# Performance work log

Hardware: AMD Instinct MI355X
Metric: run time of the kernel (lower is better)

Reference implementation:

```python
import jax, jax.numpy as jnp
import numpy as np
import math

B, S, H, NH = 1, 2048, 1024, 16  # batch, seq, hidden, heads


def setup_inputs() -> dict:
    key = jax.random.key(0)
    ks = jax.random.split(key, 12)
    inp = {
        "query": jax.random.normal(ks[0], (B, S, H), dtype=jnp.float32),
        "key": jax.random.normal(ks[1], (B, S, H), dtype=jnp.float32),
        "value": jax.random.normal(ks[2], (B, S, H), dtype=jnp.float32),
        "attention_mask": jax.random.randint(ks[3], (1, 1, S, S), 0, 2, dtype=jnp.int32),
        # torch nn.Linear params: y = x @ W.T + b, W init ~ U(-1/sqrt(H), 1/sqrt(H))
        "Wq": jax.random.uniform(ks[4], (H, H), jnp.float32, -1, 1) / math.sqrt(H),
        "bq": jax.random.uniform(ks[5], (H,), jnp.float32, -1, 1) / math.sqrt(H),
        "Wk": jax.random.uniform(ks[6], (H, H), jnp.float32, -1, 1) / math.sqrt(H),
        "bk": jax.random.uniform(ks[7], (H,), jnp.float32, -1, 1) / math.sqrt(H),
        "Wv": jax.random.uniform(ks[8], (H, H), jnp.float32, -1, 1) / math.sqrt(H),
        "bv": jax.random.uniform(ks[9], (H,), jnp.float32, -1, 1) / math.sqrt(H),
        "Wo": jax.random.uniform(ks[10], (H, H), jnp.float32, -1, 1) / math.sqrt(H),
        "bo": jax.random.uniform(ks[11], (H,), jnp.float32, -1, 1) / math.sqrt(H),
        "head": NH,
        "hidden_size": H,
    }
    return inp


def reference(query, key, value, attention_mask, Wq, bq, Wk, bk, Wv, bv, Wo, bo, head, hidden_size):
    b, s, _ = query.shape
    d_k = hidden_size // head

    def proj(x, W, bias):
        # [b, s, hidden] -> [b, head, s, d_k]
        y = x @ W.T + bias
        return y.reshape(b, s, head, d_k).transpose(0, 2, 1, 3)

    q = proj(query, Wq, bq)
    k = proj(key, Wk, bk)
    v = proj(value, Wv, bv)

    # naive full score matrix, as in the source (scale by sqrt(d_k) = last dim of q)
    scores = jnp.einsum("bhqd,bhkd->bhqk", q, k) / math.sqrt(d_k)
    # faithful quirk: masked positions are set to 0 (not -inf) before softmax
    scores = jnp.where(attention_mask == 0, jnp.zeros((), scores.dtype), scores)
    attn = jax.nn.softmax(scores, axis=-1)

    out = jnp.einsum("bhqk,bhkd->bhqd", attn, v)  # [b, head, s, d_k]
    out = out.transpose(0, 2, 1, 3).reshape(b, s, head * d_k)
    return out @ Wo.T + bo
```

## Files before the change

kernel.cpp:

```cpp
#include <hip/hip_runtime.h>
#include <hip/hip_bf16.h>


#define S_LEN 2048
#define HID   1024
#define NHEAD 16
#define DK    64

typedef unsigned short u16;
typedef __attribute__((ext_vector_type(8))) short bf16x8;
typedef __attribute__((ext_vector_type(4))) short bf16x4;
typedef __attribute__((ext_vector_type(4))) float f32x4;
typedef __attribute__((ext_vector_type(4))) unsigned u32x4;

__device__ __forceinline__ void load16_lds(const void* g, void* l) {
  __builtin_amdgcn_global_load_lds(
      (const __attribute__((address_space(1))) void*)g,
      (__attribute__((address_space(3))) void*)l, 16, 0, 0);
}

__device__ __forceinline__ short bfbits(float x) {
  __hip_bfloat16 h = __float2bfloat16(x);
  return *(short*)&h;
}
__device__ __forceinline__ bf16x8 cvt8(float4 a, float4 b) {
  bf16x8 r;
  r[0] = bfbits(a.x); r[1] = bfbits(a.y); r[2] = bfbits(a.z); r[3] = bfbits(a.w);
  r[4] = bfbits(b.x); r[5] = bfbits(b.y); r[6] = bfbits(b.z); r[7] = bfbits(b.w);
  return r;
}
__device__ __forceinline__ float bf2f(u16 u) {
  unsigned v = (unsigned)u << 16;
  return *(float*)&v;
}

__global__ __launch_bounds__(256) void cvt_kernel(
    const float* __restrict__ q, const float* __restrict__ k,
    const float* __restrict__ v, const float* __restrict__ wq,
    const float* __restrict__ wk, const float* __restrict__ wv,
    const float* __restrict__ wo, u16* __restrict__ Xbf,
    u16* __restrict__ Wbf) {
  const int y = blockIdx.y;
  size_t i = ((size_t)blockIdx.x * 256 + threadIdx.x) * 8;
  const float* src;
  u16* dst;
  size_t n;
  if (y < 3) {
    src = y == 0 ? q : (y == 1 ? k : v);
    dst = Xbf + (size_t)y * (S_LEN * HID);
    n = (size_t)S_LEN * HID;
  } else {
    int w = y - 3;
    src = w == 0 ? wq : (w == 1 ? wk : (w == 2 ? wv : wo));
    dst = Wbf + (size_t)w * (HID * HID);
    n = (size_t)HID * HID;
  }
  if (i >= n) return;
  float4 a = *(const float4*)(src + i);
  float4 b = *(const float4*)(src + i + 4);
  *(bf16x8*)(dst + i) = cvt8(a, b);
}

__global__ __launch_bounds__(256) void pack_mask_kernel(
    const int* __restrict__ mask, unsigned int* __restrict__ bitsT) {
  int idx = blockIdx.x * 256 + threadIdx.x;
  int row = idx & 2047, widx = idx >> 11;
  const int4* p = (const int4*)(mask + (size_t)row * S_LEN + widx * 32);
  unsigned word = 0;
#pragma unroll
  for (int i = 0; i < 8; ++i) {
    int4 v = p[i];
    word |= (unsigned)(v.x != 0) << (i * 4 + 0);
    word |= (unsigned)(v.y != 0) << (i * 4 + 1);
    word |= (unsigned)(v.z != 0) << (i * 4 + 2);
    word |= (unsigned)(v.w != 0) << (i * 4 + 3);
  }
  bitsT[(size_t)widx * S_LEN + row] = word;
}

__global__ __launch_bounds__(256) void gemm_qkv(
    const u16* __restrict__ Xbf, const u16* __restrict__ Wbf,
    const float* __restrict__ bq, const float* __restrict__ bk,
    const float* __restrict__ bv, u16* __restrict__ Qb,
    u16* __restrict__ Kb, u16* __restrict__ Vt) {
  constexpr int Mm = 2048, Nn = 1024, Kk = 1024, NIT = 16;
  const int z = blockIdx.z;
  const u16* A = Xbf + (size_t)z * (S_LEN * HID);
  const u16* W = Wbf + (size_t)z * (HID * HID);
  const float* bias = z == 0 ? bq : (z == 1 ? bk : bv);
  u16* C = z == 0 ? Qb : (z == 1 ? Kb : Vt);
  const float oscale = (z == 0) ? 0.125f * 1.44269504088896f : 1.0f;
  const int transpose = (z == 2);

  const int tid = threadIdx.x, lane = tid & 63, wave = tid >> 6;
  const int q4 = lane >> 4, c16 = lane & 15;
  const int bx = blockIdx.x;
  const int mBase = (bx & 31) * 64;
  const int nBase = (bx >> 5) * 128;
  const int wn = wave * 32;

  __shared__ __align__(16) u16 As[2][2][64 * 32];
  __shared__ __align__(16) u16 Bs[2][2][128 * 32];

  f32x4 acc[4][2] = {};
  const int srow = lane >> 2, se8 = (lane & 3) * 8;

  auto issue = [&](int it, int buf) {
#pragma unroll
    for (int j = 0; j < 2; ++j) {
      int u = wave * 2 + j, h = u >> 2, grp = u & 3;
      load16_lds(A + (size_t)(mBase + grp * 16 + srow) * Kk + it * 64 +
                     h * 32 + se8,
                 &As[buf][h][grp * 512]);
    }
#pragma unroll
    for (int j = 0; j < 4; ++j) {
      int u = wave * 4 + j, h = u >> 3, grp = u & 7;
      load16_lds(W + (size_t)(nBase + grp * 16 + srow) * Kk + it * 64 +
                     h * 32 + se8,
                 &Bs[buf][h][grp * 512]);
    }
  };

  issue(0, 0);
  __syncthreads();

  for (int it = 0; it < NIT; ++it) {
    const int buf = it & 1, nbuf = buf ^ 1;
    if (it + 1 < NIT) issue(it + 1, nbuf);
#pragma unroll
    for (int kk = 0; kk < 2; ++kk) {
      bf16x8 af[4], bfr[2];
#pragma unroll
      for (int t = 0; t < 4; ++t)
        af[t] = *(const bf16x8*)&As[buf][kk][(t * 16 + c16) * 32 + q4 * 8];
#pragma unroll
      for (int t = 0; t < 2; ++t)
        bfr[t] = *(const bf16x8*)&Bs[buf][kk][(wn + t * 16 + c16) * 32 + q4 * 8];
#pragma unroll
      for (int mt = 0; mt < 4; ++mt)
#pragma unroll
        for (int nt = 0; nt < 2; ++nt)
          acc[mt][nt] = __builtin_amdgcn_mfma_f32_16x16x32_bf16(
              af[mt], bfr[nt], acc[mt][nt], 0, 0, 0);
    }
    __syncthreads();
  }

#pragma unroll
  for (int nt = 0; nt < 2; ++nt) {
    int col = nBase + wn + nt * 16 + c16;
    float bv2 = bias[col];
#pragma unroll
    for (int mt = 0; mt < 4; ++mt) {
#pragma unroll
      for (int r = 0; r < 4; ++r) {
        int row = mBase + mt * 16 + q4 * 4 + r;
        float v = (acc[mt][nt][r] + bv2) * oscale;
        if (transpose)
          ((__hip_bfloat16*)C)[(size_t)col * Mm + row] = __float2bfloat16(v);
        else
          ((__hip_bfloat16*)C)[(size_t)row * Nn + col] = __float2bfloat16(v);
      }
    }
  }
}

__global__ __launch_bounds__(512, 4) void attn_kernel(
    const u16* __restrict__ Qb, const u16* __restrict__ Kb,
    const u16* __restrict__ Vt, const unsigned* __restrict__ mbT,
    u16* __restrict__ partOA, u16* __restrict__ partO3,
    float* __restrict__ partL) {
  constexpr int NITA = 8;
  const int qt = blockIdx.x, h = blockIdx.y, zz = blockIdx.z;
  const int tid = threadIdx.x, lane = tid & 63, wave = tid >> 6;
  const int q4 = lane >> 4, c16 = lane & 15;

  __shared__ __align__(16) u16 Ks[2][2][64 * 32];
  __shared__ __align__(16) u16 Vs[2][2][64 * 32];
  __shared__ __align__(16) u16 Ps[8][32 * 72];

  const int q0 = qt * 256 + wave * 32;

  bf16x8 qf[2][2];
#pragma unroll
  for (int m = 0; m < 2; ++m)
#pragma unroll
    for (int kk = 0; kk < 2; ++kk)
      qf[m][kk] = *(const bf16x8*)(Qb + (size_t)(q0 + m * 16 + c16) * HID +
                                   h * DK + kk * 32 + q4 * 8);

  f32x4 o[2][4] = {};
  float l_lane[2][4] = {{}, {}};
  const unsigned mlo = 1u << c16, mhi = mlo << 16;

  const int srow = lane >> 2;
  const int sslot = ((lane & 3) ^ (srow & 3)) * 8;
  const int kvbase = zz * (S_LEN / 4);

  auto issueKV = [&](int it, int buf) {
    const int kv0 = kvbase + it * 64;
#pragma unroll
    for (int j = 0; j < 2; ++j) {
      int i = wave * 2 + j;
      if (i < 8) {
        int half = i >> 2, grp = i & 3;
        load16_lds(Kb + (size_t)(kv0 + grp * 16 + srow) * HID + h * DK +
                       half * 32 + sslot,
                   &Ks[buf][half][grp * 512]);
      } else {
        int ii = i - 8;
        int half = ii >> 2, grp = ii & 3;
        load16_lds(Vt + (size_t)(h * DK + grp * 16 + srow) * S_LEN + kv0 +
                       half * 32 + sslot,
                   &Vs[buf][half][grp * 512]);
      }
    }
  };

  issueKV(0, 0);
  __syncthreads();

  __hip_bfloat16* pw = (__hip_bfloat16*)&Ps[wave][0];

  for (int it = 0; it < NITA; ++it) {
    const int buf = it & 1, nbuf = buf ^ 1;
    if (it + 1 < NITA) issueKV(it + 1, nbuf);

    const unsigned* mr = mbT + (size_t)(zz * 16 + it * 2) * S_LEN + q0 + q4 * 4;
    u32x4 mwa[2][2];
#pragma unroll
    for (int m = 0; m < 2; ++m) {
      mwa[m][0] = *(const u32x4*)(mr + m * 16);
      mwa[m][1] = *(const u32x4*)(mr + S_LEN + m * 16);
    }

#pragma unroll
    for (int nt = 0; nt < 4; ++nt) {
      const int rsw = (nt * 16 + c16) * 32 + ((q4 ^ (c16 & 3)) * 8);
      bf16x8 kf0 = *(const bf16x8*)&Ks[buf][0][rsw];
      bf16x8 kf1 = *(const bf16x8*)&Ks[buf][1][rsw];
#pragma unroll
      for (int m = 0; m < 2; ++m) {
        f32x4 a = {};
        a = __builtin_amdgcn_mfma_f32_16x16x32_bf16(qf[m][0], kf0, a, 0, 0, 0);
        a = __builtin_amdgcn_mfma_f32_16x16x32_bf16(qf[m][1], kf1, a, 0, 0, 0);
#pragma unroll
        for (int r = 0; r < 4; ++r) {
          unsigned word = mwa[m][nt >> 1][r];
          unsigned keep = word & ((nt & 1) ? mhi : mlo);
          float s = keep ? a[r] : 0.0f;
          float p = exp2f(s);
          l_lane[m][r] += p;
          pw[(m * 16 + q4 * 4 + r) * 72 + nt * 16 + c16] = __float2bfloat16(p);
        }
      }
    }

    asm volatile("s_waitcnt lgkmcnt(0)" ::: "memory");

#pragma unroll
    for (int kk = 0; kk < 2; ++kk) {
      bf16x8 pa0 = *(const bf16x8*)&Ps[wave][(c16) * 72 + kk * 32 + q4 * 8];
      bf16x8 pa1 = *(const bf16x8*)&Ps[wave][(16 + c16) * 72 + kk * 32 + q4 * 8];
#pragma unroll
      for (int nt = 0; nt < 4; ++nt) {
        const int rsw = (nt * 16 + c16) * 32 + ((q4 ^ (c16 & 3)) * 8);
        bf16x8 vb = *(const bf16x8*)&Vs[buf][kk][rsw];
        o[0][nt] = __builtin_amdgcn_mfma_f32_16x16x32_bf16(pa0, vb, o[0][nt], 0, 0, 0);
        o[1][nt] = __builtin_amdgcn_mfma_f32_16x16x32_bf16(pa1, vb, o[1][nt], 0, 0, 0);
      }
    }
    __syncthreads();
  }

  u16* pO = (zz < 3) ? (partOA + (size_t)zz * (S_LEN * HID)) : partO3;
#pragma unroll
  for (int m = 0; m < 2; ++m)
#pragma unroll
    for (int r = 0; r < 4; ++r) {
      float s = l_lane[m][r];
#pragma unroll
      for (int d = 1; d < 16; d <<= 1) s += __shfl_xor(s, d);
      int row = q0 + m * 16 + q4 * 4 + r;
#pragma unroll
      for (int nt = 0; nt < 4; ++nt)
        ((__hip_bfloat16*)pO)[(size_t)row * HID + h * DK + nt * 16 + c16] =
            __float2bfloat16(o[m][nt][r]);
      if (c16 == 0)
        partL[((size_t)zz * NHEAD + h) * S_LEN + row] = s;
    }
}

__global__ __launch_bounds__(256) void combine_kernel(
    const u16* __restrict__ pOA, const u16* __restrict__ pO3,
    const float* __restrict__ partL, u16* __restrict__ ctx) {
  size_t idx = ((size_t)blockIdx.x * 256 + threadIdx.x) * 4;
  int row = (int)(idx >> 10);
  int col = (int)(idx & 1023);
  int h = col >> 6;
  float l = 0.0f;
#pragma unroll
  for (int z = 0; z < 4; ++z)
    l += partL[((size_t)z * NHEAD + h) * S_LEN + row];
  float inv = 1.0f / l;
  bf16x4 a0 = *(const bf16x4*)(pOA + idx);
  bf16x4 a1 = *(const bf16x4*)(pOA + (size_t)S_LEN * HID + idx);
  bf16x4 a2 = *(const bf16x4*)(pOA + 2 * (size_t)S_LEN * HID + idx);
  bf16x4 a3 = *(const bf16x4*)(pO3 + idx);
  bf16x4 r;
#pragma unroll
  for (int j = 0; j < 4; ++j) {
    float v = (bf2f((u16)a0[j]) + bf2f((u16)a1[j]) + bf2f((u16)a2[j]) +
               bf2f((u16)a3[j])) * inv;
    r[j] = bfbits(v);
  }
  *(bf16x4*)(ctx + idx) = r;
}

__global__ __launch_bounds__(256) void gemm_out(
    const u16* __restrict__ ctx, const u16* __restrict__ Wo,
    const float* __restrict__ bo, float* __restrict__ out) {
  constexpr int Nn = 1024, Kk = 1024, NIT = 16;
  const int tid = threadIdx.x, lane = tid & 63, wave = tid >> 6;
  const int q4 = lane >> 4, c16 = lane & 15;
  const int bx = blockIdx.x;
  const int mBase = (bx & 63) * 32;
  const int nBase = (bx >> 6) * 128;
  const int wn = wave * 32;

  __shared__ __align__(16) u16 As[2][2][32 * 32];
  __shared__ __align__(16) u16 Bs[2][2][128 * 32];

  f32x4 acc[2][2] = {};
  const int srow = lane >> 2, se8 = (lane & 3) * 8;

  auto issue = [&](int it, int buf) {
    {
      int u = wave, h = u >> 1, grp = u & 1;
      load16_lds(ctx + (size_t)(mBase + grp * 16 + srow) * Kk + it * 64 +
                     h * 32 + se8,
                 &As[buf][h][grp * 512]);
    }
#pragma unroll
    for (int j = 0; j < 4; ++j) {
      int u = wave * 4 + j, h = u >> 3, grp = u & 7;
      load16_lds(Wo + (size_t)(nBase + grp * 16 + srow) * Kk + it * 64 +
                     h * 32 + se8,
                 &Bs[buf][h][grp * 512]);
    }
  };

  issue(0, 0);
  __syncthreads();

  for (int it = 0; it < NIT; ++it) {
    const int buf = it & 1, nbuf = buf ^ 1;
    if (it + 1 < NIT) issue(it + 1, nbuf);
#pragma unroll
    for (int kk = 0; kk < 2; ++kk) {
      bf16x8 af[2], bfr[2];
#pragma unroll
      for (int t = 0; t < 2; ++t)
        af[t] = *(const bf16x8*)&As[buf][kk][(t * 16 + c16) * 32 + q4 * 8];
#pragma unroll
      for (int t = 0; t < 2; ++t)
        bfr[t] = *(const bf16x8*)&Bs[buf][kk][(wn + t * 16 + c16) * 32 + q4 * 8];
#pragma unroll
      for (int mt = 0; mt < 2; ++mt)
#pragma unroll
        for (int nt = 0; nt < 2; ++nt)
          acc[mt][nt] = __builtin_amdgcn_mfma_f32_16x16x32_bf16(
              af[mt], bfr[nt], acc[mt][nt], 0, 0, 0);
    }
    __syncthreads();
  }

#pragma unroll
  for (int nt = 0; nt < 2; ++nt) {
    int col = nBase + wn + nt * 16 + c16;
    float bv = bo[col];
#pragma unroll
    for (int mt = 0; mt < 2; ++mt)
#pragma unroll
      for (int r = 0; r < 4; ++r) {
        int row = mBase + mt * 16 + q4 * 4 + r;
        out[(size_t)row * Nn + col] = acc[mt][nt][r] + bv;
      }
  }
}

extern "C" void kernel_launch(void* const* d_in, const int* in_sizes, int n_in,
                              void* d_out, int out_size, void* d_ws, size_t ws_size,
                              hipStream_t stream) {
  const float* q    = (const float*)d_in[0];
  const float* k    = (const float*)d_in[1];
  const float* v    = (const float*)d_in[2];
  const int*   mask = (const int*)d_in[3];
  const float* Wq = (const float*)d_in[4];
  const float* bq = (const float*)d_in[5];
  const float* Wk = (const float*)d_in[6];
  const float* bk = (const float*)d_in[7];
  const float* Wv = (const float*)d_in[8];
  const float* bv = (const float*)d_in[9];
  const float* Wo = (const float*)d_in[10];
  const float* bo = (const float*)d_in[11];

  const size_t M2 = (size_t)S_LEN * HID;
  const size_t W1 = (size_t)HID * HID;
  const size_t need = (4 * W1 + 3 * M2 + 3 * M2) * 2 +
                      (size_t)S_LEN * 64 * 4 + 2 * NHEAD * S_LEN * 4;
  if (ws_size < need) return;

  u16* Wbf = (u16*)d_ws;
  u16* Xbf = Wbf + 4 * W1;
  u16* Qb = Xbf + 3 * M2;
  u16* Kb = Qb + M2;
  u16* Vt = Kb + M2;
  unsigned* mbits = (unsigned*)(Vt + M2);
  u16* partOA = Xbf;
  u16* partO3 = Wbf;
  float* partL = (float*)(Wbf + 2 * W1);
  u16* ctx = Qb;

  hipLaunchKernelGGL(cvt_kernel, dim3(1024, 7), dim3(256), 0, stream,
                     q, k, v, Wq, Wk, Wv, Wo, Xbf, Wbf);

  hipLaunchKernelGGL(pack_mask_kernel, dim3((S_LEN * (S_LEN / 32)) / 256),
                     dim3(256), 0, stream, mask, mbits);

  hipLaunchKernelGGL(gemm_qkv, dim3(256, 1, 3), dim3(256), 0, stream,
                     Xbf, Wbf, bq, bk, bv, Qb, Kb, Vt);

  hipLaunchKernelGGL(attn_kernel, dim3(S_LEN / 256, NHEAD, 4), dim3(512), 0,
                     stream, Qb, Kb, Vt, mbits, partOA, partO3, partL);

  hipLaunchKernelGGL(combine_kernel, dim3((S_LEN * HID / 4) / 256), dim3(256),
                     0, stream, partOA, partO3, partL, ctx);

  hipLaunchKernelGGL(gemm_out, dim3(512), dim3(256), 0, stream,
                     ctx, Wbf + 3 * W1, bo, (float*)d_out);
}
```

Measured before the change: 227.0 us.

## Swizzle LDS tiles, remap blocks per XCD, pack P stores with permuted V

Changes the LDS XOR swizzle in the QKV, output and attention kernels to key on (row>>1), so 16-byte fragment reads hit fewer bank conflicts. Remaps block indices in all three kernels so blocks on the same XCD share A/W or K/V tiles in that XCD's L2. In attention, the score-to-P write is restructured to emit packed 32-bit bf16 pairs instead of scattered 16-bit stores. To keep that correct, the V^T output of the QKV GEMM is written with a matching interleaved row permutation within each 32-key group. The added index arithmetic and the coupled layout across kernels raise the risk of subtle correctness mismatches.

```diff
diff --git a/kernel.cpp b/kernel.cpp
--- a/kernel.cpp
+++ b/kernel.cpp
@@ -95,29 +95,32 @@
   const int tid = threadIdx.x, lane = tid & 63, wave = tid >> 6;
   const int q4 = lane >> 4, c16 = lane & 15;
   const int bx = blockIdx.x;
-  const int mBase = (bx & 31) * 64;
-  const int nBase = (bx >> 5) * 128;
+  const int xcd = bx & 7, sIdx = bx >> 3;
+  const int mBase = ((xcd >> 1) * 8 + (sIdx & 7)) * 64;
+  const int nBase = ((xcd & 1) * 4 + (sIdx >> 3)) * 128;
   const int wn = wave * 32;
 
   __shared__ __align__(16) u16 As[2][2][64 * 32];
   __shared__ __align__(16) u16 Bs[2][2][128 * 32];
 
   f32x4 acc[4][2] = {};
-  const int srow = lane >> 2, se8 = (lane & 3) * 8;
+  const int srow = lane >> 2;
+  const int sx8 = ((lane & 3) ^ ((srow >> 1) & 3)) * 8;
+  const int rx8 = (q4 ^ ((c16 >> 1) & 3)) * 8;
 
   auto issue = [&](int it, int buf) {
 #pragma unroll
     for (int j = 0; j < 2; ++j) {
       int u = wave * 2 + j, h = u >> 2, grp = u & 3;
       load16_lds(A + (size_t)(mBase + grp * 16 + srow) * Kk + it * 64 +
-                     h * 32 + se8,
+                     h * 32 + sx8,
                  &As[buf][h][grp * 512]);
     }
 #pragma unroll
     for (int j = 0; j < 4; ++j) {
       int u = wave * 4 + j, h = u >> 3, grp = u & 7;
       load16_lds(W + (size_t)(nBase + grp * 16 + srow) * Kk + it * 64 +
-                     h * 32 + se8,
+                     h * 32 + sx8,
                  &Bs[buf][h][grp * 512]);
     }
   };
@@ -133,10 +136,10 @@
       bf16x8 af[4], bfr[2];
 #pragma unroll
       for (int t = 0; t < 4; ++t)
-        af[t] = *(const bf16x8*)&As[buf][kk][(t * 16 + c16) * 32 + q4 * 8];
+        af[t] = *(const bf16x8*)&As[buf][kk][(t * 16 + c16) * 32 + rx8];
 #pragma unroll
       for (int t = 0; t < 2; ++t)
-        bfr[t] = *(const bf16x8*)&Bs[buf][kk][(wn + t * 16 + c16) * 32 + q4 * 8];
+        bfr[t] = *(const bf16x8*)&Bs[buf][kk][(wn + t * 16 + c16) * 32 + rx8];
 #pragma unroll
       for (int mt = 0; mt < 4; ++mt)
 #pragma unroll
@@ -157,10 +160,13 @@
       for (int r = 0; r < 4; ++r) {
         int row = mBase + mt * 16 + q4 * 4 + r;
         float v = (acc[mt][nt][r] + bv2) * oscale;
-        if (transpose)
-          ((__hip_bfloat16*)C)[(size_t)col * Mm + row] = __float2bfloat16(v);
-        else
+        if (transpose) {
+          int vv = row & 31;
+          int rowp = (row & ~31) | (((vv & 15) << 1) | (vv >> 4));
+          ((__hip_bfloat16*)C)[(size_t)col * Mm + rowp] = __float2bfloat16(v);
+        } else {
           ((__hip_bfloat16*)C)[(size_t)row * Nn + col] = __float2bfloat16(v);
+        }
       }
     }
   }
@@ -172,7 +178,9 @@
     u16* __restrict__ partOA, u16* __restrict__ partO3,
     float* __restrict__ partL) {
   constexpr int NITA = 8;
-  const int qt = blockIdx.x, h = blockIdx.y, zz = blockIdx.z;
+  const int lin = blockIdx.x + 8 * (blockIdx.y + 16 * blockIdx.z);
+  const int work = ((lin & 7) << 6) | (lin >> 3);
+  const int qt = work & 7, h = (work >> 3) & 15, zz = work >> 7;
   const int tid = threadIdx.x, lane = tid & 63, wave = tid >> 6;
   const int q4 = lane >> 4, c16 = lane & 15;
 
@@ -195,7 +203,8 @@
   const unsigned mlo = 1u << c16, mhi = mlo << 16;
 
   const int srow = lane >> 2;
-  const int sslot = ((lane & 3) ^ (srow & 3)) * 8;
+  const int sx8 = ((lane & 3) ^ ((srow >> 1) & 3)) * 8;
+  const int rx8 = (q4 ^ ((c16 >> 1) & 3)) * 8;
   const int kvbase = zz * (S_LEN / 4);
 
   auto issueKV = [&](int it, int buf) {
@@ -206,13 +215,13 @@
       if (i < 8) {
         int half = i >> 2, grp = i & 3;
         load16_lds(Kb + (size_t)(kv0 + grp * 16 + srow) * HID + h * DK +
-                       half * 32 + sslot,
+                       half * 32 + sx8,
                    &Ks[buf][half][grp * 512]);
       } else {
         int ii = i - 8;
         int half = ii >> 2, grp = ii & 3;
         load16_lds(Vt + (size_t)(h * DK + grp * 16 + srow) * S_LEN + kv0 +
-                       half * 32 + sslot,
+                       half * 32 + sx8,
                    &Vs[buf][half][grp * 512]);
       }
     }
@@ -221,7 +230,7 @@
   issueKV(0, 0);
   __syncthreads();
 
-  __hip_bfloat16* pw = (__hip_bfloat16*)&Ps[wave][0];
+  u16* pw = &Ps[wave][0];
 
   for (int it = 0; it < NITA; ++it) {
     const int buf = it & 1, nbuf = buf ^ 1;
@@ -235,9 +244,10 @@
       mwa[m][1] = *(const u32x4*)(mr + S_LEN + m * 16);
     }
 
+    f32x4 sv[2][4];
 #pragma unroll
     for (int nt = 0; nt < 4; ++nt) {
-      const int rsw = (nt * 16 + c16) * 32 + ((q4 ^ (c16 & 3)) * 8);
+      const int rsw = (nt * 16 + c16) * 32 + rx8;
       bf16x8 kf0 = *(const bf16x8*)&Ks[buf][0][rsw];
       bf16x8 kf1 = *(const bf16x8*)&Ks[buf][1][rsw];
 #pragma unroll
@@ -245,27 +255,41 @@
         f32x4 a = {};
         a = __builtin_amdgcn_mfma_f32_16x16x32_bf16(qf[m][0], kf0, a, 0, 0, 0);
         a = __builtin_amdgcn_mfma_f32_16x16x32_bf16(qf[m][1], kf1, a, 0, 0, 0);
-#pragma unroll
-        for (int r = 0; r < 4; ++r) {
+        sv[m][nt] = a;
+      }
+    }
+
+#pragma unroll
+    for (int m = 0; m < 2; ++m)
+#pragma unroll
+      for (int r = 0; r < 4; ++r) {
+#pragma unroll
+        for (int nt = 0; nt < 4; ++nt) {
           unsigned word = mwa[m][nt >> 1][r];
           unsigned keep = word & ((nt & 1) ? mhi : mlo);
-          float s = keep ? a[r] : 0.0f;
+          float s = keep ? sv[m][nt][r] : 0.0f;
           float p = exp2f(s);
+          sv[m][nt][r] = p;
           l_lane[m][r] += p;
-          pw[(m * 16 + q4 * 4 + r) * 72 + nt * 16 + c16] = __float2bfloat16(p);
         }
-      }
-    }
+        int prow = m * 16 + q4 * 4 + r;
+#pragma unroll
+        for (int kkp = 0; kkp < 2; ++kkp) {
+          unsigned lo = (unsigned)(u16)bfbits(sv[m][2 * kkp][r]);
+          unsigned hi = (unsigned)(u16)bfbits(sv[m][2 * kkp + 1][r]);
+          *(unsigned*)&pw[prow * 72 + kkp * 32 + c16 * 2] = lo | (hi << 16);
+        }
+      }
 
     asm volatile("s_waitcnt lgkmcnt(0)" ::: "memory");
 
 #pragma unroll
     for (int kk = 0; kk < 2; ++kk) {
-      bf16x8 pa0 = *(const bf16x8*)&Ps[wave][(c16) * 72 + kk * 32 + q4 * 8];
-      bf16x8 pa1 = *(const bf16x8*)&Ps[wave][(16 + c16) * 72 + kk * 32 + q4 * 8];
+      bf16x8 pa0 = *(const bf16x8*)&pw[(c16) * 72 + kk * 32 + q4 * 8];
+      bf16x8 pa1 = *(const bf16x8*)&pw[(16 + c16) * 72 + kk * 32 + q4 * 8];
 #pragma unroll
       for (int nt = 0; nt < 4; ++nt) {
-        const int rsw = (nt * 16 + c16) * 32 + ((q4 ^ (c16 & 3)) * 8);
+        const int rsw = (nt * 16 + c16) * 32 + rx8;
         bf16x8 vb = *(const bf16x8*)&Vs[buf][kk][rsw];
         o[0][nt] = __builtin_amdgcn_mfma_f32_16x16x32_bf16(pa0, vb, o[0][nt], 0, 0, 0);
         o[1][nt] = __builtin_amdgcn_mfma_f32_16x16x32_bf16(pa1, vb, o[1][nt], 0, 0, 0);
@@ -325,28 +349,31 @@
   const int tid = threadIdx.x, lane = tid & 63, wave = tid >> 6;
   const int q4 = lane >> 4, c16 = lane & 15;
   const int bx = blockIdx.x;
-  const int mBase = (bx & 63) * 32;
-  const int nBase = (bx >> 6) * 128;
+  const int xcd = bx & 7, sIdx = bx >> 3;
+  const int mBase = ((xcd >> 1) * 16 + (sIdx & 15)) * 32;
+  const int nBase = ((xcd & 1) * 4 + (sIdx >> 4)) * 128;
   const int wn = wave * 32;
 
   __shared__ __align__(16) u16 As[2][2][32 * 32];
   __shared__ __align__(16) u16 Bs[2][2][128 * 32];
 
   f32x4 acc[2][2] = {};
-  const int srow = lane >> 2, se8 = (lane & 3) * 8;
+  const int srow = lane >> 2;
+  const int sx8 = ((lane & 3) ^ ((srow >> 1) & 3)) * 8;
+  const int rx8 = (q4 ^ ((c16 >> 1) & 3)) * 8;
 
   auto issue = [&](int it, int buf) {
     {
       int u = wave, h = u >> 1, grp = u & 1;
       load16_lds(ctx + (size_t)(mBase + grp * 16 + srow) * Kk + it * 64 +
-                     h * 32 + se8,
+                     h * 32 + sx8,
                  &As[buf][h][grp * 512]);
     }
 #pragma unroll
     for (int j = 0; j < 4; ++j) {
       int u = wave * 4 + j, h = u >> 3, grp = u & 7;
       load16_lds(Wo + (size_t)(nBase + grp * 16 + srow) * Kk + it * 64 +
-                     h * 32 + se8,
+                     h * 32 + sx8,
                  &Bs[buf][h][grp * 512]);
     }
   };
@@ -362,10 +389,10 @@
       bf16x8 af[2], bfr[2];
 #pragma unroll
       for (int t = 0; t < 2; ++t)
-        af[t] = *(const bf16x8*)&As[buf][kk][(t * 16 + c16) * 32 + q4 * 8];
+        af[t] = *(const bf16x8*)&As[buf][kk][(t * 16 + c16) * 32 + rx8];
 #pragma unroll
       for (int t = 0; t < 2; ++t)
-        bfr[t] = *(const bf16x8*)&Bs[buf][kk][(wn + t * 16 + c16) * 32 + q4 * 8];
+        bfr[t] = *(const bf16x8*)&Bs[buf][kk][(wn + t * 16 + c16) * 32 + rx8];
 #pragma unroll
       for (int mt = 0; mt < 2; ++mt)
 #pragma unroll
```

Result: faster. 206.6 us (-9.0%).
